# Kernel tuning notes

Hardware: AMD Instinct MI355X
Metric: run time of the kernel (lower is better)

Reference implementation:

```python
import jax, jax.numpy as jnp
import numpy as np

BN_EPS = 1e-5
NN_EPS = 1e-8


def _conv_bn_relu(x, w, gamma, beta, mean, var):
    # x: (B, Cin, N), w: (Cout, Cin) -- 1x1 Conv1d (no bias) + BatchNorm1d (eval) + ReLU
    y = jnp.einsum('oc,bcn->bon', w, x)
    scale = gamma / jnp.sqrt(var + BN_EPS)            # (Cout,)
    shift = beta - mean * scale                       # (Cout,)
    return jax.nn.relu(y * scale[:, None] + shift[:, None])


def setup_inputs() -> dict:
    key = jax.random.key(0)
    ks = jax.random.split(key, 10)
    B, N, M = 4, 2048, 8192
    Cin, Cout = 512, 256
    inp = {
        'x1': jax.random.normal(ks[0], (B, Cin, N), dtype=jnp.float32),
        'p1': jax.random.uniform(ks[1], (B, N, 3), dtype=jnp.float32) * 4.0,
        'x2': jax.random.normal(ks[2], (B, Cout, M), dtype=jnp.float32),
        'p2': jax.random.uniform(ks[3], (B, M, 3), dtype=jnp.float32) * 4.0,
        # up_mlp params
        'w_up': jax.random.normal(ks[4], (Cout, Cin), dtype=jnp.float32) * (1.0 / np.sqrt(Cin)),
        'g_up': jnp.ones((Cout,), jnp.float32),
        'b_up': jnp.zeros((Cout,), jnp.float32),
        'm_up': jax.random.normal(ks[5], (Cout,), dtype=jnp.float32) * 0.1,
        'v_up': jax.random.uniform(ks[6], (Cout,), dtype=jnp.float32) + 0.5,
        # lateral_mlp params
        'w_lat': jax.random.normal(ks[7], (Cout, Cout), dtype=jnp.float32) * (1.0 / np.sqrt(Cout)),
        'g_lat': jnp.ones((Cout,), jnp.float32),
        'b_lat': jnp.zeros((Cout,), jnp.float32),
        'm_lat': jax.random.normal(ks[8], (Cout,), dtype=jnp.float32) * 0.1,
        'v_lat': jax.random.uniform(ks[9], (Cout,), dtype=jnp.float32) + 0.5,
    }
    return inp


def reference(x1, p1, x2, p2, w_up, g_up, b_up, m_up, v_up,
              w_lat, g_lat, b_lat, m_lat, v_lat):
    # up branch: conv1x1 + BN + ReLU on coarse features  (B, Cout, N)
    f1 = _conv_bn_relu(x1, w_up, g_up, b_up, m_up, v_up)

    # three_nn: for each fine point p2 find 3 nearest coarse points p1 (squared dist)
    d2 = (jnp.sum(p2 * p2, -1)[:, :, None]
          + jnp.sum(p1 * p1, -1)[:, None, :]
          - 2.0 * jnp.einsum('bmd,bnd->bmn', p2, p1))        # (B, M, N)
    d2 = jnp.maximum(d2, 0.0)
    neg_d, idx = jax.lax.top_k(-d2, 3)                       # (B, M, 3)
    dist = -neg_d

    # inverse-distance weights
    dist_recip = 1.0 / (dist + NN_EPS)
    weight = dist_recip / jnp.sum(dist_recip, axis=2, keepdims=True)  # (B, M, 3)

    # three_interpolate: gather + weighted sum
    gathered = jax.vmap(lambda f, i: f[:, i])(f1, idx)       # (B, Cout, M, 3)
    interp = jnp.einsum('bcmk,bmk->bcm', gathered, weight)   # (B, Cout, M)

    # lateral branch
    f2 = _conv_bn_relu(x2, w_lat, g_lat, b_lat, m_lat, v_lat)

    return interp + f2, p2
```

## Files before the change

### kernel.cpp

```cpp
#include <hip/hip_runtime.h>
#include <math.h>
#include <float.h>

#define B_    4
#define N_    2048
#define M_    8192
#define CIN_  512
#define COUT_ 256

typedef __attribute__((ext_vector_type(8))) short short8v;
typedef __attribute__((ext_vector_type(4))) float f32x4;

__device__ __forceinline__ void ws_store_f32(float* p, float v) {
    __hip_atomic_store((unsigned int*)p, __float_as_uint(v),
                       __ATOMIC_RELAXED, __HIP_MEMORY_SCOPE_SYSTEM);
}
__device__ __forceinline__ void ws_store_u32(int* p, int v) {
    __hip_atomic_store((unsigned int*)p, (unsigned int)v,
                       __ATOMIC_RELAXED, __HIP_MEMORY_SCOPE_SYSTEM);
}

__global__ __launch_bounds__(64) void inv_kernel() {
    asm volatile("buffer_inv sc0 sc1" ::: "memory");
}

__device__ __forceinline__ unsigned short f2bf(float f) {
    unsigned u = __float_as_uint(f);
    u += 0x7fffu + ((u >> 16) & 1u);
    return (unsigned short)(u >> 16);
}

template<int K, int MODE>
__device__ __forceinline__ void gemm_body(
    char* raw, int b, int c0, int m0,
    const float* __restrict__ X, const float* __restrict__ W,
    const float* __restrict__ gam, const float* __restrict__ bet,
    const float* __restrict__ mu, const float* __restrict__ var,
    float* __restrict__ dst,
    const float* __restrict__ f1t, const float* __restrict__ nnrec, int Mdim)
{
    char* Ab = raw;
    char* Bb = raw + 5120;

    const int tid = threadIdx.x;
    const int l  = tid & 63;
    const int wv = tid >> 6;
    const int wc = wv & 1, wn = wv >> 1;

    f32x4 acc[2][4];
    #pragma unroll
    for (int i = 0; i < 2; ++i)
        #pragma unroll
        for (int j = 0; j < 4; ++j)
            acc[i][j] = (f32x4){0.f, 0.f, 0.f, 0.f};

    const int ksA = tid & 7;
    const int crA = tid >> 3;
    const int kqB = tid >> 5;
    const int mlB = tid & 31;

    float4 ra[4]; float2 rb[4];
    if constexpr (MODE == 1) {
        #pragma unroll
        for (int ni = 0; ni < 4; ++ni) {
            int mg = m0 + wn * 64 + ni * 16 + (l & 15);
            const float* rp = nnrec + ((size_t)b * M_ + mg) * 8;
            ra[ni] = *(const float4*)rp;
            rb[ni] = *(const float2*)(rp + 4);
        }
    }

    float4 wreg[2];
    float  xreg[4][4];
    #pragma unroll
    for (int r = 0; r < 2; ++r)
        wreg[r] = *(const float4*)(W + (size_t)(c0 + crA + 32 * r) * K + ksA * 4);
    #pragma unroll
    for (int jj = 0; jj < 4; ++jj) {
        const float* xp = X + ((size_t)b * K + kqB * 4) * Mdim + m0 + mlB + 32 * jj;
        xreg[jj][0] = xp[0];
        xreg[jj][1] = xp[(size_t)Mdim];
        xreg[jj][2] = xp[(size_t)2 * Mdim];
        xreg[jj][3] = xp[(size_t)3 * Mdim];
    }

    for (int kc = 0; kc < K; kc += 32) {
        #pragma unroll
        for (int r = 0; r < 2; ++r) {
            unsigned lo = f2bf(wreg[r].x) | ((unsigned)f2bf(wreg[r].y) << 16);
            unsigned hi = f2bf(wreg[r].z) | ((unsigned)f2bf(wreg[r].w) << 16);
            *(uint2*)(Ab + (crA + 32 * r) * 80 + ksA * 8) = make_uint2(lo, hi);
        }
        #pragma unroll
        for (int jj = 0; jj < 4; ++jj) {
            unsigned lo = f2bf(xreg[jj][0]) | ((unsigned)f2bf(xreg[jj][1]) << 16);
            unsigned hi = f2bf(xreg[jj][2]) | ((unsigned)f2bf(xreg[jj][3]) << 16);
            *(uint2*)(Bb + (mlB + 32 * jj) * 80 + kqB * 8) = make_uint2(lo, hi);
        }
        if (kc + 32 < K) {
            #pragma unroll
            for (int r = 0; r < 2; ++r)
                wreg[r] = *(const float4*)(W + (size_t)(c0 + crA + 32 * r) * K + (kc + 32) + ksA * 4);
            #pragma unroll
            for (int jj = 0; jj < 4; ++jj) {
                const float* xp = X + ((size_t)b * K + (kc + 32) + kqB * 4) * Mdim + m0 + mlB + 32 * jj;
                xreg[jj][0] = xp[0];
                xreg[jj][1] = xp[(size_t)Mdim];
                xreg[jj][2] = xp[(size_t)2 * Mdim];
                xreg[jj][3] = xp[(size_t)3 * Mdim];
            }
        }
        __syncthreads();
        short8v a[2], bfv[4];
        #pragma unroll
        for (int ci = 0; ci < 2; ++ci)
            a[ci] = *(const short8v*)(Ab + (wc * 32 + ci * 16 + (l & 15)) * 80 + (l >> 4) * 16);
        #pragma unroll
        for (int ni = 0; ni < 4; ++ni)
            bfv[ni] = *(const short8v*)(Bb + (wn * 64 + ni * 16 + (l & 15)) * 80 + (l >> 4) * 16);
        #pragma unroll
        for (int ci = 0; ci < 2; ++ci)
            #pragma unroll
            for (int ni = 0; ni < 4; ++ni)
                acc[ci][ni] = __builtin_amdgcn_mfma_f32_16x16x32_bf16(
                    a[ci], bfv[ni], acc[ci][ni], 0, 0, 0);
        __syncthreads();
    }

    const int lc = (l >> 4) * 4;
    float scA[2][4], shA[2][4];
    #pragma unroll
    for (int ci = 0; ci < 2; ++ci)
        #pragma unroll
        for (int r = 0; r < 4; ++r) {
            int c = c0 + wc * 32 + ci * 16 + lc + r;
            float sc = gam[c] / sqrtf(var[c] + 1e-5f);
            scA[ci][r] = sc;
            shA[ci][r] = bet[c] - mu[c] * sc;
        }

    if constexpr (MODE == 0) {
        float* S = (float*)raw;
        #pragma unroll
        for (int h = 0; h < 2; ++h) {
            if (wn == h) {
                #pragma unroll
                for (int ni = 0; ni < 4; ++ni)
                    #pragma unroll
                    for (int ci = 0; ci < 2; ++ci)
                        #pragma unroll
                        for (int r = 0; r < 4; ++r)
                            S[(ni * 16 + (l & 15)) * 66 + wc * 32 + ci * 16 + lc + r] =
                                fmaxf(acc[ci][ni][r] * scA[ci][r] + shA[ci][r], 0.f);
            }
            __syncthreads();
            #pragma unroll
            for (int i = 0; i < 16; ++i) {
                int e = tid + i * 256;
                int row = e >> 6, c = e & 63;
                ws_store_f32(dst + ((size_t)b * N_ + m0 + h * 64 + row) * COUT_ + c0 + c,
                             S[row * 66 + c]);
            }
            __syncthreads();
        }
    } else {
        #pragma unroll
        for (int ni = 0; ni < 4; ++ni) {
            int mg = m0 + wn * 64 + ni * 16 + (l & 15);
            int   i0 = __float_as_int(ra[ni].x);
            int   i1 = __float_as_int(ra[ni].y);
            int   i2 = __float_as_int(ra[ni].z);
            float w0 = ra[ni].w, w1 = rb[ni].x, w2 = rb[ni].y;
            const float4* g0 = (const float4*)(f1t + ((size_t)b * N_ + i0) * COUT_ + c0 + wc * 32 + lc);
            const float4* g1 = (const float4*)(f1t + ((size_t)b * N_ + i1) * COUT_ + c0 + wc * 32 + lc);
            const float4* g2 = (const float4*)(f1t + ((size_t)b * N_ + i2) * COUT_ + c0 + wc * 32 + lc);
            #pragma unroll
            for (int ci = 0; ci < 2; ++ci) {
                float4 G0 = g0[ci * 4];
                float4 G1 = g1[ci * 4];
                float4 G2 = g2[ci * 4];
                const float* f0 = (const float*)&G0;
                const float* f1 = (const float*)&G1;
                const float* f2 = (const float*)&G2;
                #pragma unroll
                for (int r = 0; r < 4; ++r) {
                    float v = fmaxf(acc[ci][ni][r] * scA[ci][r] + shA[ci][r], 0.f);
                    v = fmaf(w0, f0[r], v);
                    v = fmaf(w1, f1[r], v);
                    v = fmaf(w2, f2[r], v);
                    int c = c0 + wc * 32 + ci * 16 + lc + r;
                    dst[((size_t)b * COUT_ + c) * M_ + mg] = v;
                }
            }
        }
    }
}

__global__ __launch_bounds__(256) void up_kernel(
    const float* __restrict__ x1, const float* __restrict__ w_up,
    const float* __restrict__ g_up, const float* __restrict__ b_up,
    const float* __restrict__ m_up, const float* __restrict__ v_up,
    float* __restrict__ f1t)
{
    __shared__ float4 raw4[1056];
    gemm_body<CIN_, 0>((char*)raw4, blockIdx.z, blockIdx.y * 64, blockIdx.x * 128,
                       x1, w_up, g_up, b_up, m_up, v_up, f1t,
                       nullptr, nullptr, N_);
}

__global__ __launch_bounds__(256) void lat_kernel(
    const float* __restrict__ x2, const float* __restrict__ w_lat,
    const float* __restrict__ g_lat, const float* __restrict__ b_lat,
    const float* __restrict__ m_lat, const float* __restrict__ v_lat,
    const float* __restrict__ f1t, const float* __restrict__ nnrec,
    float* __restrict__ out0)
{
    __shared__ float4 raw4[960];
    gemm_body<COUT_, 1>((char*)raw4, blockIdx.z, blockIdx.y * 64, blockIdx.x * 128,
                        x2, w_lat, g_lat, b_lat, m_lat, v_lat, out0,
                        f1t, nnrec, M_);
}

__device__ __forceinline__ void lex_insert(float e, int j,
    float& D0, float& D1, float& D2, int& I0, int& I1, int& I2)
{
    bool l0 = (e < D0) || (e == D0 && j < I0);
    bool l1 = (e < D1) || (e == D1 && j < I1);
    bool l2 = (e < D2) || (e == D2 && j < I2);
    if (l2) {
        if (l0)      { D2=D1; I2=I1; D1=D0; I1=I0; D0=e; I0=j; }
        else if (l1) { D2=D1; I2=I1; D1=e;  I1=j; }
        else         { D2=e;  I2=j; }
    }
}

__device__ __forceinline__ void bubble_insert(float e, int ie,
    float& D0, float& D1, float& D2, int& I0, int& I1, int& I2)
{
    bool l2 = e < D2;
    D2 = l2 ? e  : D2;
    I2 = l2 ? ie : I2;
    bool s1 = D2 < D1;
    float tf = D1; int ti = I1;
    D1 = s1 ? D2 : D1;  I1 = s1 ? I2 : I1;
    D2 = s1 ? tf : D2;  I2 = s1 ? ti : I2;
    bool s0 = D1 < D0;
    tf = D0; ti = I0;
    D0 = s0 ? D1 : D0;  I0 = s0 ? I1 : I0;
    D1 = s0 ? tf : D1;  I1 = s0 ? ti : I1;
}

__global__ __launch_bounds__(256) void three_nn_kernel(
    const float* __restrict__ p1, const float* __restrict__ p2,
    float* __restrict__ nnrec, float* __restrict__ out1)
{
    __shared__ float4 P[8][257];
    const int b = blockIdx.y;
    #pragma unroll
    for (int r = 0; r < 8; ++r) {
        int n = r * 256 + threadIdx.x;
        float x = p1[((size_t)(b*N_)+n)*3 + 0];
        float y = p1[((size_t)(b*N_)+n)*3 + 1];
        float z = p1[((size_t)(b*N_)+n)*3 + 2];
        float t = x * x;
        t = fmaf(y, y, t);
        t = fmaf(z, z, t);
        P[r][threadIdx.x] = make_float4(x, y, z, t);
    }
    __syncthreads();

    const int m = blockIdx.x * 32 + (threadIdx.x >> 3);
    const int s = threadIdx.x & 7;
    const size_t pbase = ((size_t)(b*M_) + m) * 3;
    const float qx = p2[pbase+0], qy = p2[pbase+1], qz = p2[pbase+2];
    float s2 = qx * qx;
    s2 = fmaf(qy, qy, s2);
    s2 = fmaf(qz, qz, s2);

    float D0 = FLT_MAX, D1 = FLT_MAX, D2 = FLT_MAX;
    int   I0 = 0x7fffffff, I1 = 0x7fffffff, I2 = 0x7fffffff;
    const int base = s * 256;
    const float4* Ps = &P[s][0];

    float4 ca[8], cb[8];
    #pragma unroll
    for (int u = 0; u < 8; ++u) ca[u] = Ps[u];

    #define PROC(CV, IB)                                                     \
        {                                                                    \
            float d[8];                                                      \
            _Pragma("unroll")                                                \
            for (int u = 0; u < 8; ++u) {                                    \
                float dot = qx * CV[u].x;                                    \
                dot = fmaf(qy, CV[u].y, dot);                                \
                dot = fmaf(qz, CV[u].z, dot);                                \
                float d2 = fmaf(-2.0f, dot, s2 + CV[u].w);                   \
                d[u] = fmaxf(d2, 0.0f);                                      \
            }                                                                \
            _Pragma("unroll")                                                \
            for (int u = 0; u < 8; ++u)                                      \
                bubble_insert(d[u], (IB) + u, D0, D1, D2, I0, I1, I2);       \
        }

    for (int j = 0; j < 32; j += 2) {
        #pragma unroll
        for (int u = 0; u < 8; ++u) cb[u] = Ps[(j + 1) * 8 + u];
        PROC(ca, base + j * 8);
        if (j + 2 < 32) {
            #pragma unroll
            for (int u = 0; u < 8; ++u) ca[u] = Ps[(j + 2) * 8 + u];
        }
        PROC(cb, base + (j + 1) * 8);
    }
    #undef PROC

    #pragma unroll
    for (int st = 1; st <= 4; st <<= 1) {
        float E0 = __shfl_xor(D0, st), E1 = __shfl_xor(D1, st), E2 = __shfl_xor(D2, st);
        int   J0 = __shfl_xor(I0, st), J1 = __shfl_xor(I1, st), J2 = __shfl_xor(I2, st);
        lex_insert(E0, J0, D0, D1, D2, I0, I1, I2);
        lex_insert(E1, J1, D0, D1, D2, I0, I1, I2);
        lex_insert(E2, J2, D0, D1, D2, I0, I1, I2);
    }
    if (s == 0) {
        float r0 = 1.0f / (D0 + 1e-8f);
        float r1 = 1.0f / (D1 + 1e-8f);
        float r2 = 1.0f / (D2 + 1e-8f);
        float sum = (r0 + r1) + r2;
        float* rp = nnrec + ((size_t)(b*M_) + m) * 8;
        ws_store_u32((int*)rp + 0, I0);
        ws_store_u32((int*)rp + 1, I1);
        ws_store_u32((int*)rp + 2, I2);
        ws_store_f32(rp + 3, r0 / sum);
        ws_store_f32(rp + 4, r1 / sum);
        ws_store_f32(rp + 5, r2 / sum);
        size_t o = ((size_t)(b*M_) + m) * 3;
        out1[o+0] = qx; out1[o+1] = qy; out1[o+2] = qz;
    }
}

extern "C" void kernel_launch(void* const* d_in, const int* in_sizes, int n_in,
                              void* d_out, int out_size, void* d_ws, size_t ws_size,
                              hipStream_t stream)
{
    (void)in_sizes; (void)n_in; (void)out_size; (void)ws_size;

    const float* x1    = (const float*)d_in[0];
    const float* p1    = (const float*)d_in[1];
    const float* x2    = (const float*)d_in[2];
    const float* p2    = (const float*)d_in[3];
    const float* w_up  = (const float*)d_in[4];
    const float* g_up  = (const float*)d_in[5];
    const float* b_up  = (const float*)d_in[6];
    const float* m_up  = (const float*)d_in[7];
    const float* v_up  = (const float*)d_in[8];
    const float* w_lat = (const float*)d_in[9];
    const float* g_lat = (const float*)d_in[10];
    const float* b_lat = (const float*)d_in[11];
    const float* m_lat = (const float*)d_in[12];
    const float* v_lat = (const float*)d_in[13];

    float* out0 = (float*)d_out;
    float* out1 = out0 + (size_t)B_ * COUT_ * M_;

    float* f1t   = (float*)d_ws;
    float* nnrec = f1t + (size_t)B_ * N_ * COUT_;

    up_kernel<<<dim3(N_ / 128, COUT_ / 64, B_), 256, 0, stream>>>(
        x1, w_up, g_up, b_up, m_up, v_up, f1t);

    three_nn_kernel<<<dim3(M_ / 32, B_), 256, 0, stream>>>(
        p1, p2, nnrec, out1);

    inv_kernel<<<dim3(512), 64, 0, stream>>>();

    lat_kernel<<<dim3(M_ / 128, COUT_ / 64, B_), 256, 0, stream>>>(
        x2, w_lat, g_lat, b_lat, m_lat, v_lat, f1t, nnrec, out0);
}
```

Baseline: 94.00 us.

## Split three-NN scan across 16 lanes per query and use min/max insertion

The three_nn kernel now uses 512 threads per block, with 16 lanes per query point each scanning 128 candidates instead of 8 lanes scanning 256. The reduction adds one more shuffle stage. The top-3 insert is rewritten as a min/max network with predicated index selects, which shortens the dependent chain of compare/swap steps. The aim is a shorter serial latency per thread and more parallelism, at the cost of an extra merge stage and a block size that may limit occupancy. Tie handling in the insert is unchanged: equal distances still do not replace.

Result: slower. 104.5 us (+11.2%).

```diff
diff --git a/kernel.cpp b/kernel.cpp
--- a/kernel.cpp
+++ b/kernel.cpp
@@ -234,43 +234,46 @@
     }
 }
 
-__device__ __forceinline__ void bubble_insert(float e, int ie,
+__device__ __forceinline__ void mm_insert(float d, int iv,
     float& D0, float& D1, float& D2, int& I0, int& I1, int& I2)
 {
-    bool l2 = e < D2;
-    D2 = l2 ? e  : D2;
-    I2 = l2 ? ie : I2;
-    bool s1 = D2 < D1;
-    float tf = D1; int ti = I1;
-    D1 = s1 ? D2 : D1;  I1 = s1 ? I2 : I1;
-    D2 = s1 ? tf : D2;  I2 = s1 ? ti : I2;
-    bool s0 = D1 < D0;
-    tf = D0; ti = I0;
-    D0 = s0 ? D1 : D0;  I0 = s0 ? I1 : I0;
-    D1 = s0 ? tf : D1;  I1 = s0 ? ti : I1;
-}
-
-__global__ __launch_bounds__(256) void three_nn_kernel(
+    bool c1 = d < D0;
+    bool c2 = d < D1;
+    bool c3 = d < D2;
+    int nI2 = c3 ? (c2 ? I1 : iv) : I2;
+    int nI1 = c2 ? (c1 ? I0 : iv) : I1;
+    int nI0 = c1 ? iv : I0;
+    float t   = fmaxf(D0, d);
+    float nD0 = fminf(D0, d);
+    float nD1 = fminf(D1, t);
+    float t2  = fmaxf(D1, t);
+    float nD2 = fminf(D2, t2);
+    D0 = nD0; D1 = nD1; D2 = nD2;
+    I0 = nI0; I1 = nI1; I2 = nI2;
+}
+
+__global__ __launch_bounds__(512) void three_nn_kernel(
     const float* __restrict__ p1, const float* __restrict__ p2,
     float* __restrict__ nnrec, float* __restrict__ out1)
 {
-    __shared__ float4 P[8][257];
+    __shared__ float4 P[16][129];
     const int b = blockIdx.y;
-    #pragma unroll
-    for (int r = 0; r < 8; ++r) {
-        int n = r * 256 + threadIdx.x;
+    const int tid = threadIdx.x;
+    #pragma unroll
+    for (int r = 0; r < 4; ++r) {
+        int n = r * 512 + tid;
         float x = p1[((size_t)(b*N_)+n)*3 + 0];
         float y = p1[((size_t)(b*N_)+n)*3 + 1];
         float z = p1[((size_t)(b*N_)+n)*3 + 2];
         float t = x * x;
         t = fmaf(y, y, t);
         t = fmaf(z, z, t);
-        P[r][threadIdx.x] = make_float4(x, y, z, t);
+        P[n >> 7][n & 127] = make_float4(x, y, z, t);
     }
     __syncthreads();
 
-    const int m = blockIdx.x * 32 + (threadIdx.x >> 3);
-    const int s = threadIdx.x & 7;
+    const int m = blockIdx.x * 32 + (tid >> 4);
+    const int s = tid & 15;
     const size_t pbase = ((size_t)(b*M_) + m) * 3;
     const float qx = p2[pbase+0], qy = p2[pbase+1], qz = p2[pbase+2];
     float s2 = qx * qx;
@@ -279,7 +282,7 @@
 
     float D0 = FLT_MAX, D1 = FLT_MAX, D2 = FLT_MAX;
     int   I0 = 0x7fffffff, I1 = 0x7fffffff, I2 = 0x7fffffff;
-    const int base = s * 256;
+    const int base = s * 128;
     const float4* Ps = &P[s][0];
 
     float4 ca[8], cb[8];
@@ -299,14 +302,14 @@
             }                                                                \
             _Pragma("unroll")                                                \
             for (int u = 0; u < 8; ++u)                                      \
-                bubble_insert(d[u], (IB) + u, D0, D1, D2, I0, I1, I2);       \
-        }
-
-    for (int j = 0; j < 32; j += 2) {
+                mm_insert(d[u], (IB) + u, D0, D1, D2, I0, I1, I2);           \
+        }
+
+    for (int j = 0; j < 16; j += 2) {
         #pragma unroll
         for (int u = 0; u < 8; ++u) cb[u] = Ps[(j + 1) * 8 + u];
         PROC(ca, base + j * 8);
-        if (j + 2 < 32) {
+        if (j + 2 < 16) {
             #pragma unroll
             for (int u = 0; u < 8; ++u) ca[u] = Ps[(j + 2) * 8 + u];
         }
@@ -315,7 +318,7 @@
     #undef PROC
 
     #pragma unroll
-    for (int st = 1; st <= 4; st <<= 1) {
+    for (int st = 1; st <= 8; st <<= 1) {
         float E0 = __shfl_xor(D0, st), E1 = __shfl_xor(D1, st), E2 = __shfl_xor(D2, st);
         int   J0 = __shfl_xor(I0, st), J1 = __shfl_xor(I1, st), J2 = __shfl_xor(I2, st);
         lex_insert(E0, J0, D0, D1, D2, I0, I1, I2);
@@ -369,7 +372,7 @@
     up_kernel<<<dim3(N_ / 128, COUT_ / 64, B_), 256, 0, stream>>>(
         x1, w_up, g_up, b_up, m_up, v_up, f1t);
 
-    three_nn_kernel<<<dim3(M_ / 32, B_), 256, 0, stream>>>(
+    three_nn_kernel<<<dim3(M_ / 32, B_), 512, 0, stream>>>(
         p1, p2, nnrec, out1);
 
     inv_kernel<<<dim3(512), 64, 0, stream>>>();
```
